# Performance work log

Measured on AMD Instinct MI355X. Metric: run time of the kernel, lower is better.

Reference implementation:

```python
import jax, jax.numpy as jnp
import numpy as np
from jax import lax

B, CIN, L, COUT, K = 64, 64, 4096, 128, 7
STRIDE, PAD = 1, 3
POOL, POOL_STRIDE = 2, 2
BN_EPS = 1e-5


def setup_inputs() -> dict:
    key = jax.random.key(0)
    ks = jax.random.split(key, 7)
    I = jax.random.normal(ks[0], (B, CIN, L), jnp.float32)
    bn_gamma = 1.0 + 0.1 * jax.random.normal(ks[1], (CIN,), jnp.float32)
    bn_beta = 0.1 * jax.random.normal(ks[2], (CIN,), jnp.float32)
    bn_mean = 0.1 * jax.random.normal(ks[3], (CIN,), jnp.float32)
    bn_var = jax.random.uniform(ks[4], (CIN,), jnp.float32, 0.5, 1.5)
    conv_w = 0.05 * jax.random.normal(ks[5], (COUT, CIN, K), jnp.float32)
    # XNOR-Net style per-output-channel scale alpha = mean(|W|) over (Cin, K)
    alpha = jnp.mean(jnp.abs(conv_w), axis=(1, 2))  # [COUT]
    prelu_w = jnp.full((1,), 0.25, jnp.float32)  # nn.PReLU() default: 1 shared param
    return dict(I=I, bn_gamma=bn_gamma, bn_beta=bn_beta, bn_mean=bn_mean,
                bn_var=bn_var, conv_w=conv_w, alpha=alpha, prelu_w=prelu_w)


def reference(I, bn_gamma, bn_beta, bn_mean, bn_var, conv_w, alpha, prelu_w):
    # BatchNorm1d (eval mode: running stats), per-channel over dim 1
    scale = (bn_gamma / jnp.sqrt(bn_var + BN_EPS))[None, :, None]
    x = (I - bn_mean[None, :, None]) * scale + bn_beta[None, :, None]
    # Binarize (sign; sign(0)=0 matches torch.sign)
    x = jnp.sign(x)
    # Conv1d, no bias, zero padding=3, stride=1  -> [B, COUT, L]
    y = lax.conv_general_dilated(x, conv_w, window_strides=(STRIDE,),
                                 padding=[(PAD, PAD)],
                                 dimension_numbers=('NCH', 'OIH', 'NCH'))
    # alpha scale (per output channel)
    y = y * alpha[None, :, None]
    # PReLU with single shared parameter
    y = jnp.where(y > 0, y, prelu_w[0] * y)
    # MaxPool1d(kernel=2, stride=2)
    y = lax.reduce_window(y, -jnp.inf, lax.max,
                          (1, 1, POOL), (1, 1, POOL_STRIDE), 'VALID')
    return y
```

## Files before the change

### kernel.cpp

```cpp
#include <hip/hip_runtime.h>
#include <hip/hip_bf16.h>
#include <stdint.h>

#define BATCH 64
#define CIN   64
#define LEN   4096
#define COUT  128
#define KW    7
#define LPOOL 2048
#define NT    4
#define RROWS 72
#define RAWP  80

typedef __bf16 v8bf __attribute__((ext_vector_type(8)));
typedef unsigned short v8us __attribute__((ext_vector_type(8)));
typedef float  v4f  __attribute__((ext_vector_type(4)));

typedef const __attribute__((address_space(1))) void* gp1_t;
typedef __attribute__((address_space(3))) void* lp3_t;

__global__ __launch_bounds__(256)
void wconv_kernel(const float* __restrict__ W, ushort* __restrict__ Wt) {
    int i = blockIdx.x * 256 + threadIdx.x;
    if (i >= COUT * CIN * KW) return;
    int co  = i / (CIN * KW);
    int rem = i - co * (CIN * KW);
    int ci  = rem / KW;
    int k   = rem - ci * KW;
    uint u = __float_as_uint(W[i]);
    uint r = (u + 0x7FFFu + ((u >> 16) & 1u)) >> 16;
    Wt[(k * COUT + co) * CIN + ci] = (ushort)r;
}

__global__ __launch_bounds__(256, 4)
void conv_kernel(const float* __restrict__ I,
                 const float* __restrict__ bn_g, const float* __restrict__ bn_b,
                 const float* __restrict__ bn_m, const float* __restrict__ bn_v,
                 const ushort* __restrict__ Wt,
                 const float* __restrict__ alpha, const float* __restrict__ prelu,
                 float* __restrict__ out) {
    __shared__ __attribute__((aligned(16))) float  raw[CIN * RAWP];
    __shared__ __attribute__((aligned(16))) ushort stg[RROWS * 72];
    __shared__ float4 bnc[CIN];

    int tid = threadIdx.x;
    int lane = tid & 63, wave = tid >> 6;
    int b = blockIdx.y, bx = blockIdx.x;
    int l0base = bx * (64 * NT);

    if (tid < CIN) {
        float s = __fdiv_rn(bn_g[tid], __fsqrt_rn(__fadd_rn(bn_v[tid], 1e-5f)));
        bnc[tid] = make_float4(s, bn_m[tid], bn_b[tid], 0.f);
    }

    const float* Ib = I + (size_t)b * CIN * LEN;

    const char* gb[5]; int cb[5];
    #pragma unroll
    for (int i = 0; i < 5; ++i) {
        int n = (wave * 5 + i) * 64 + lane;
        int ci = n / 20;
        int c  = n - 20 * ci;
        cb[i] = 16 * c - 32;
        gb[i] = (const char*)(Ib + (size_t)ci * LEN) + cb[i];
    }

    {
        int l4 = 4 * l0base;
        #pragma unroll
        for (int i = 0; i < 5; ++i) {
            int off = cb[i] + l4;
            if (off >= 0 && off + 16 <= LEN * 4)
                __builtin_amdgcn_global_load_lds((gp1_t)(gb[i] + l4),
                                                 (lp3_t)(raw + (wave * 5 + i) * 256), 16, 0, 0);
        }
    }
    __syncthreads();

    int g8 = tid >> 5, rb = tid & 31;
    int quad = lane >> 4, lr = lane & 15;
    int cout0 = wave * 32;
    const ushort* wbase = Wt + ((size_t)cout0 + lr) * CIN + quad * 8;
    float pw  = prelu[0];
    float al0 = alpha[cout0 + lr];
    float al1 = alpha[cout0 + 16 + lr];
    float* obase = out + ((size_t)b * COUT) * LPOOL + bx * (32 * NT);

    for (int t = 0; t < NT; ++t) {
        int l0 = l0base + t * 64;

        #pragma unroll
        for (int it = 0; it < 3; ++it) {
            int r = rb + 32 * it;
            if (r < RROWS) {
                int p = l0 - 4 + r;
                bool pok = (p >= 0) && (p < LEN);
                v8us u;
                #pragma unroll
                for (int j = 0; j < 8; ++j) {
                    float4 cc = bnc[8 * g8 + j];
                    float v = raw[(8 * g8 + j) * RAWP + r + 4];
                    float x = __fadd_rn(__fmul_rn(__fsub_rn(v, cc.y), cc.x), cc.z);
                    ushort s = x > 0.f ? (ushort)0x3F80 : (x < 0.f ? (ushort)0xBF80 : (ushort)0);
                    u[j] = pok ? s : (ushort)0;
                }
                *(v8us*)(&stg[r * 72 + g8 * 8]) = u;
            }
        }
        __syncthreads();

        if (t + 1 < NT) {
            int l4 = 4 * (l0 + 64);
            #pragma unroll
            for (int i = 0; i < 5; ++i) {
                int off = cb[i] + l4;
                if (off >= 0 && off + 16 <= LEN * 4)
                    __builtin_amdgcn_global_load_lds((gp1_t)(gb[i] + l4),
                                                     (lp3_t)(raw + (wave * 5 + i) * 256), 16, 0, 0);
            }
        }

        v4f acc[4][2];
        #pragma unroll
        for (int mt = 0; mt < 4; ++mt) { acc[mt][0] = (v4f)0.f; acc[mt][1] = (v4f)0.f; }

        const ushort* wk   = wbase;
        const ushort* arow = &stg[(lr + 1) * 72 + quad * 8];
        #pragma unroll 1
        for (int k = 0; k < KW; ++k) {
            v8bf w00 = *(const v8bf*)(wk);
            v8bf w01 = *(const v8bf*)(wk + 16 * CIN);
            v8bf w10 = *(const v8bf*)(wk + 32);
            v8bf w11 = *(const v8bf*)(wk + 32 + 16 * CIN);
            #pragma unroll
            for (int mt = 0; mt < 4; ++mt) {
                v8bf a0 = *(const v8bf*)(arow + mt * 16 * 72);
                v8bf a1 = *(const v8bf*)(arow + mt * 16 * 72 + 32);
                acc[mt][0] = __builtin_amdgcn_mfma_f32_16x16x32_bf16(a0, w00, acc[mt][0], 0, 0, 0);
                acc[mt][1] = __builtin_amdgcn_mfma_f32_16x16x32_bf16(a0, w01, acc[mt][1], 0, 0, 0);
                acc[mt][0] = __builtin_amdgcn_mfma_f32_16x16x32_bf16(a1, w10, acc[mt][0], 0, 0, 0);
                acc[mt][1] = __builtin_amdgcn_mfma_f32_16x16x32_bf16(a1, w11, acc[mt][1], 0, 0, 0);
            }
            wk   += COUT * CIN;
            arow += 72;
        }

        float* ob = obase + t * 32;
        #pragma unroll
        for (int n2 = 0; n2 < 2; ++n2) {
            float al = n2 ? al1 : al0;
            int co = cout0 + n2 * 16 + lr;
            float* oc = ob + (size_t)co * LPOOL + quad * 2;
            #pragma unroll
            for (int mt = 0; mt < 4; ++mt) {
                float v0 = acc[mt][n2][0] * al; v0 = v0 > 0.f ? v0 : pw * v0;
                float v1 = acc[mt][n2][1] * al; v1 = v1 > 0.f ? v1 : pw * v1;
                float v2 = acc[mt][n2][2] * al; v2 = v2 > 0.f ? v2 : pw * v2;
                float v3 = acc[mt][n2][3] * al; v3 = v3 > 0.f ? v3 : pw * v3;
                *(float2*)(oc + mt * 8) = make_float2(fmaxf(v0, v1), fmaxf(v2, v3));
            }
        }
        __syncthreads();
    }
}

extern "C" void kernel_launch(void* const* d_in, const int* in_sizes, int n_in,
                              void* d_out, int out_size, void* d_ws, size_t ws_size,
                              hipStream_t stream) {
    const float* I      = (const float*)d_in[0];
    const float* bn_g   = (const float*)d_in[1];
    const float* bn_b   = (const float*)d_in[2];
    const float* bn_m   = (const float*)d_in[3];
    const float* bn_v   = (const float*)d_in[4];
    const float* conv_w = (const float*)d_in[5];
    const float* alpha  = (const float*)d_in[6];
    const float* prelu  = (const float*)d_in[7];
    float* out = (float*)d_out;

    ushort* Wt = (ushort*)d_ws;

    wconv_kernel<<<(COUT * CIN * KW + 255) / 256, 256, 0, stream>>>(conv_w, Wt);
    dim3 grid(LEN / (64 * NT), BATCH);
    conv_kernel<<<grid, 256, 0, stream>>>(I, bn_g, bn_b, bn_m, bn_v, Wt, alpha, prelu, out);
}
```

Measured before the change: 177.2 us.

## Swizzle staging LDS layout, vectorize binarize, prefetch weights across taps

Replaces the padded 72-pitch bf16 staging buffer with a 64-pitch XOR-swizzled layout meant to avoid LDS bank conflicts on the MFMA A-operand reads. Binarization now runs on 144 threads that each hold their 8 channels' BN constants in registers and read float4 vectors from the raw tile, dropping the shared bnc table. Weight fragments for the next kernel tap are software-prefetched into registers during the current tap's MFMAs, hiding global-load latency. Launch bounds drop from 4 to 3 waves per SIMD to make room for the extra registers, which may cost occupancy.

```diff
diff --git a/kernel.cpp b/kernel.cpp
--- a/kernel.cpp
+++ b/kernel.cpp
@@ -11,6 +11,7 @@
 #define NT    4
 #define RROWS 72
 #define RAWP  80
+#define SPITCH 64
 
 typedef __bf16 v8bf __attribute__((ext_vector_type(8)));
 typedef unsigned short v8us __attribute__((ext_vector_type(8)));
@@ -32,7 +33,7 @@
     Wt[(k * COUT + co) * CIN + ci] = (ushort)r;
 }
 
-__global__ __launch_bounds__(256, 4)
+__global__ __launch_bounds__(256, 3)
 void conv_kernel(const float* __restrict__ I,
                  const float* __restrict__ bn_g, const float* __restrict__ bn_b,
                  const float* __restrict__ bn_m, const float* __restrict__ bn_v,
@@ -40,18 +41,12 @@
                  const float* __restrict__ alpha, const float* __restrict__ prelu,
                  float* __restrict__ out) {
     __shared__ __attribute__((aligned(16))) float  raw[CIN * RAWP];
-    __shared__ __attribute__((aligned(16))) ushort stg[RROWS * 72];
-    __shared__ float4 bnc[CIN];
+    __shared__ __attribute__((aligned(16))) ushort stg[RROWS * SPITCH];
 
     int tid = threadIdx.x;
     int lane = tid & 63, wave = tid >> 6;
     int b = blockIdx.y, bx = blockIdx.x;
     int l0base = bx * (64 * NT);
-
-    if (tid < CIN) {
-        float s = __fdiv_rn(bn_g[tid], __fsqrt_rn(__fadd_rn(bn_v[tid], 1e-5f)));
-        bnc[tid] = make_float4(s, bn_m[tid], bn_b[tid], 0.f);
-    }
 
     const float* Ib = I + (size_t)b * CIN * LEN;
 
@@ -75,9 +70,21 @@
                                                  (lp3_t)(raw + (wave * 5 + i) * 256), 16, 0, 0);
         }
     }
-    __syncthreads();
-
-    int g8 = tid >> 5, rb = tid & 31;
+
+    int brq  = tid >> 3;
+    int bg8  = tid & 7;
+    int bci0 = bg8 * 8;
+    float sc[8], mn[8], bt[8];
+    if (tid < 144) {
+        #pragma unroll
+        for (int c = 0; c < 8; ++c) {
+            int ci = bci0 + c;
+            sc[c] = __fdiv_rn(bn_g[ci], __fsqrt_rn(__fadd_rn(bn_v[ci], 1e-5f)));
+            mn[c] = bn_m[ci];
+            bt[c] = bn_b[ci];
+        }
+    }
+
     int quad = lane >> 4, lr = lane & 15;
     int cout0 = wave * 32;
     const ushort* wbase = Wt + ((size_t)cout0 + lr) * CIN + quad * 8;
@@ -86,25 +93,37 @@
     float al1 = alpha[cout0 + 16 + lr];
     float* obase = out + ((size_t)b * COUT) * LPOOL + bx * (32 * NT);
 
+    v8bf c00 = *(const v8bf*)(wbase);
+    v8bf c01 = *(const v8bf*)(wbase + 16 * CIN);
+    v8bf c10 = *(const v8bf*)(wbase + 32);
+    v8bf c11 = *(const v8bf*)(wbase + 32 + 16 * CIN);
+
+    __syncthreads();
+
+    const float4* raw4 = (const float4*)raw;
+
     for (int t = 0; t < NT; ++t) {
         int l0 = l0base + t * 64;
 
-        #pragma unroll
-        for (int it = 0; it < 3; ++it) {
-            int r = rb + 32 * it;
-            if (r < RROWS) {
+        if (tid < 144) {
+            float4 fr[8];
+            #pragma unroll
+            for (int c = 0; c < 8; ++c)
+                fr[c] = raw4[(bci0 + c) * (RAWP / 4) + brq + 1];
+            #pragma unroll
+            for (int j = 0; j < 4; ++j) {
+                int r = 4 * brq + j;
                 int p = l0 - 4 + r;
                 bool pok = (p >= 0) && (p < LEN);
                 v8us u;
                 #pragma unroll
-                for (int j = 0; j < 8; ++j) {
-                    float4 cc = bnc[8 * g8 + j];
-                    float v = raw[(8 * g8 + j) * RAWP + r + 4];
-                    float x = __fadd_rn(__fmul_rn(__fsub_rn(v, cc.y), cc.x), cc.z);
+                for (int c = 0; c < 8; ++c) {
+                    float v = ((const float*)&fr[c])[j];
+                    float x = __fadd_rn(__fmul_rn(__fsub_rn(v, mn[c]), sc[c]), bt[c]);
                     ushort s = x > 0.f ? (ushort)0x3F80 : (x < 0.f ? (ushort)0xBF80 : (ushort)0);
-                    u[j] = pok ? s : (ushort)0;
+                    u[c] = pok ? s : (ushort)0;
                 }
-                *(v8us*)(&stg[r * 72 + g8 * 8]) = u;
+                *(v8us*)(&stg[r * SPITCH + ((bg8 ^ (r & 7)) << 3)]) = u;
             }
         }
         __syncthreads();
@@ -124,25 +143,29 @@
         #pragma unroll
         for (int mt = 0; mt < 4; ++mt) { acc[mt][0] = (v4f)0.f; acc[mt][1] = (v4f)0.f; }
 
-        const ushort* wk   = wbase;
-        const ushort* arow = &stg[(lr + 1) * 72 + quad * 8];
         #pragma unroll 1
         for (int k = 0; k < KW; ++k) {
-            v8bf w00 = *(const v8bf*)(wk);
-            v8bf w01 = *(const v8bf*)(wk + 16 * CIN);
-            v8bf w10 = *(const v8bf*)(wk + 32);
-            v8bf w11 = *(const v8bf*)(wk + 32 + 16 * CIN);
+            int nk = (k == KW - 1) ? 0 : k + 1;
+            const ushort* wn = wbase + nk * COUT * CIN;
+            v8bf n00 = *(const v8bf*)(wn);
+            v8bf n01 = *(const v8bf*)(wn + 16 * CIN);
+            v8bf n10 = *(const v8bf*)(wn + 32);
+            v8bf n11 = *(const v8bf*)(wn + 32 + 16 * CIN);
+
+            int rk = lr + 1 + k;
+            int s8 = rk & 7;
+            const ushort* a0p = &stg[rk * SPITCH + ((quad ^ s8) << 3)];
+            const ushort* a1p = &stg[rk * SPITCH + (((quad ^ 4) ^ s8) << 3)];
             #pragma unroll
             for (int mt = 0; mt < 4; ++mt) {
-                v8bf a0 = *(const v8bf*)(arow + mt * 16 * 72);
-                v8bf a1 = *(const v8bf*)(arow + mt * 16 * 72 + 32);
-                acc[mt][0] = __builtin_amdgcn_mfma_f32_16x16x32_bf16(a0, w00, acc[mt][0], 0, 0, 0);
-                acc[mt][1] = __builtin_amdgcn_mfma_f32_16x16x32_bf16(a0, w01, acc[mt][1], 0, 0, 0);
-                acc[mt][0] = __builtin_amdgcn_mfma_f32_16x16x32_bf16(a1, w10, acc[mt][0], 0, 0, 0);
-                acc[mt][1] = __builtin_amdgcn_mfma_f32_16x16x32_bf16(a1, w11, acc[mt][1], 0, 0, 0);
-            }
-            wk   += COUT * CIN;
-            arow += 72;
+                v8bf a0 = *(const v8bf*)(a0p + mt * 16 * SPITCH);
+                v8bf a1 = *(const v8bf*)(a1p + mt * 16 * SPITCH);
+                acc[mt][0] = __builtin_amdgcn_mfma_f32_16x16x32_bf16(a0, c00, acc[mt][0], 0, 0, 0);
+                acc[mt][1] = __builtin_amdgcn_mfma_f32_16x16x32_bf16(a0, c01, acc[mt][1], 0, 0, 0);
+                acc[mt][0] = __builtin_amdgcn_mfma_f32_16x16x32_bf16(a1, c10, acc[mt][0], 0, 0, 0);
+                acc[mt][1] = __builtin_amdgcn_mfma_f32_16x16x32_bf16(a1, c11, acc[mt][1], 0, 0, 0);
+            }
+            c00 = n00; c01 = n01; c10 = n10; c11 = n11;
         }
 
         float* ob = obase + t * 32;
```

After: 177.8 us. About the same (+0.3%).
